# Optimization experiments

Hardware: AMD Instinct MI355X
Metric: run time of the kernel (lower is better)

Reference implementation:

```python
import jax, jax.numpy as jnp
import numpy as np
from jax import lax

BETA = 0.9   # membrane decay
THR = 1.0    # firing threshold (soft reset)
K = 10       # number of time bins
# spatial pyramid for original_shape=(100,368) under 4 stride-2 SAME convs
HW = [(50, 184), (25, 92), (13, 46), (7, 23)]
CH = [4, 8, 16, 32]


def conv(x, w, b, stride=1):
    y = lax.conv_general_dilated(x, w, (stride, stride), 'SAME',
                                 dimension_numbers=('NCHW', 'OIHW', 'NCHW'))
    return y + b[None, :, None, None]


def spike(u):
    # heaviside forward, sigmoid straight-through surrogate backward
    s = (u > 0.0).astype(u.dtype)
    sg = jax.nn.sigmoid(4.0 * u)
    return sg + lax.stop_gradient(s - sg)


def setup_inputs() -> dict:
    key = jax.random.key(0)
    ks = jax.random.split(key, 12)
    T, B = 1000, 1
    x = jax.random.normal(ks[0], (T, B, 1, 100, 368), jnp.float32)

    def w(k, o, i, kh=3, kw=3):
        return 0.1 * jax.random.normal(k, (o, i, kh, kw), jnp.float32)

    inp = {'x': x}
    cin = [1] + CH[:3]
    for li in range(4):
        inp['w%d' % (li + 1)] = w(ks[1 + li], CH[li], cin[li])
        inp['b%d' % (li + 1)] = jnp.zeros((CH[li],), jnp.float32)
    sc = [2 * K * c for c in CH]  # skip channels: [80,160,320,640]
    inp['dw4'] = w(ks[5], 64, sc[3]); inp['db4'] = jnp.zeros((64,), jnp.float32)
    inp['dw3'] = w(ks[6], 32, 64 + sc[2]); inp['db3'] = jnp.zeros((32,), jnp.float32)
    inp['dw2'] = w(ks[7], 16, 32 + sc[1]); inp['db2'] = jnp.zeros((16,), jnp.float32)
    inp['dw1'] = w(ks[8], 8, 16 + sc[0]); inp['db1'] = jnp.zeros((8,), jnp.float32)
    inp['wo'] = w(ks[9], 1, 8, 1, 1); inp['bo'] = jnp.zeros((1,), jnp.float32)
    inp['total_steps'] = 1000
    inp['block_size'] = 100
    return inp


def reference(x, w1, b1, w2, b2, w3, b3, w4, b4,
              dw4, db4, dw3, db3, dw2, db2, dw1, db1, wo, bo,
              total_steps, block_size):
    S = total_steps // K  # steps per bin
    B = x.shape[1]
    xb = x.reshape((K, S) + x.shape[1:])  # [K,S,B,C,H,W]
    mems0 = tuple(jnp.zeros((B, CH[i], HW[i][0], HW[i][1]), x.dtype) for i in range(4))
    enc_w = [(w1, b1), (w2, b2), (w3, b3), (w4, b4)]

    def forward_step(x_t, mems):
        new_mems, spk = [], x_t
        for (wi, bi), m in zip(enc_w, mems):
            m = BETA * m + conv(spk, wi, bi, 2)
            spk = spike(m - THR)
            m = m - spk * THR  # soft reset
            new_mems.append(m)
        return tuple(new_mems)

    def step(carry, x_t):
        mems, sums, sqs = carry
        mems = forward_step(x_t, mems)
        sums = tuple(s + m for s, m in zip(sums, mems))
        sqs = tuple(q + m * m for q, m in zip(sqs, mems))
        return (mems, sums, sqs), None

    def bin_fn(mems, x_bin):
        zeros = tuple(jnp.zeros_like(m) for m in mems)
        (mems, sums, sqs), _ = lax.scan(step, (mems, zeros, zeros), x_bin)
        means = tuple(s / S for s in sums)
        stds = tuple(jnp.sqrt(jnp.maximum(q / S - mu * mu, 1e-8))
                     for q, mu in zip(sqs, means))
        return mems, (means, stds)

    _, (means, stds) = lax.scan(bin_fn, mems0, xb)  # each leaf: [K,B,C,H,W]

    def skip(mean, std):
        # torch.cat([mean0,std0,mean1,std1,...], dim=1) channel ordering
        f = jnp.stack([mean, std], axis=1)        # [K,2,B,C,H,W]
        f = jnp.transpose(f, (2, 0, 1, 3, 4, 5))  # [B,K,2,C,H,W]
        b_, k_, t_, c_, h_, w_ = f.shape
        return f.reshape(b_, k_ * t_ * c_, h_, w_)

    skips = [skip(means[i], stds[i]) for i in range(4)]

    def up(t, hw):
        return jax.image.resize(t, (t.shape[0], t.shape[1], hw[0], hw[1]), 'bilinear')

    relu = jax.nn.relu
    d = relu(conv(skips[3], dw4, db4))
    d = relu(conv(jnp.concatenate([up(d, HW[2]), skips[2]], 1), dw3, db3))
    d = relu(conv(jnp.concatenate([up(d, HW[1]), skips[1]], 1), dw2, db2))
    d = relu(conv(jnp.concatenate([up(d, HW[0]), skips[0]], 1), dw1, db1))
    tau_c = conv(up(d, (100, 368)), wo, bo)  # [B,1,100,368]
    return tau_c
```

## Files before the change

kernel.cpp:

```cpp
#include <hip/hip_runtime.h>

#define KBINS  10
#define SBIN   100
#define BETA   0.9f
#define THR    1.0f
#define CDIV(a,b) (((a)+(b)-1)/(b))

__global__ void k_conv1(const float* __restrict__ x,
                        const float* __restrict__ w1,
                        const float* __restrict__ b1,
                        float* __restrict__ c1) {
    int n = blockIdx.x * blockDim.x + threadIdx.x;
    if (n >= SBIN * 9200) return;
    int w   = n % 184;
    int tmp = n / 184;
    int h   = tmp % 50;
    int t   = tmp / 50;

    const float* xt = x + (size_t)t * 36800;
    float tap[9];
    #pragma unroll
    for (int kh = 0; kh < 3; kh++) {
        int r = 2 * h + kh;
        bool rok = (r < 100);
        int rc = rok ? r : 99;
        #pragma unroll
        for (int kw = 0; kw < 3; kw++) {
            int cc = 2 * w + kw;
            bool cok = (cc < 368);
            int ccc = cok ? cc : 367;
            float v = xt[rc * 368 + ccc];
            tap[kh * 3 + kw] = (rok && cok) ? v : 0.0f;
        }
    }
    float* ot = c1 + (size_t)t * 36800 + h * 184 + w;
    #pragma unroll
    for (int c = 0; c < 4; c++) {
        float acc = b1[c];
        #pragma unroll
        for (int j = 0; j < 9; j++)
            acc = fmaf(tap[j], w1[c * 9 + j], acc);
        ot[c * 9200] = acc;
    }
}

__global__ void k_scan1(const float* __restrict__ c1,
                        float* __restrict__ mstate,
                        unsigned char* __restrict__ spk,
                        float* __restrict__ skip0, int k) {
    const int PF = 10;
    int p = blockIdx.x * blockDim.x + threadIdx.x;
    if (p >= 36800) return;
    int c  = p / 9200;
    int hw = p - c * 9200;

    float m = (k == 0) ? 0.0f : mstate[p];
    float va[PF], vb[PF];
    #pragma unroll
    for (int j = 0; j < PF; j++) va[j] = c1[(size_t)j * 36800 + p];

    float s = 0.0f, q = 0.0f;
    for (int b = 0; b < SBIN / PF; b++) {
        int t0 = b * PF, tn = t0 + PF;
        bool more = (tn < SBIN);
        #pragma unroll
        for (int j = 0; j < PF; j++)
            vb[j] = more ? c1[(size_t)(tn + j) * 36800 + p] : 0.0f;
        #pragma unroll
        for (int j = 0; j < PF; j++) {
            m = fmaf(m, BETA, va[j]);
            float sp = (m - THR > 0.0f) ? 1.0f : 0.0f;
            m -= sp * THR;
            spk[(size_t)(t0 + j) * 36800 + p] = (unsigned char)sp;
            s += m;
            q = fmaf(m, m, q);
        }
        #pragma unroll
        for (int j = 0; j < PF; j++) va[j] = vb[j];
    }
    mstate[p] = m;
    float mean = s * (1.0f / SBIN);
    float var  = q * (1.0f / SBIN) - mean * mean;
    float sd   = sqrtf(fmaxf(var, 1e-8f));
    skip0[(size_t)(k * 8 + c) * 9200 + hw]     = mean;
    skip0[(size_t)(k * 8 + 4 + c) * 9200 + hw] = sd;
}

template<int CIN, int COUT, int HIN, int WIN, int HOUT, int WOUT, int PADH, int PADW>
__global__ void k_conv_s2_multi(const unsigned char* __restrict__ spk_in,
                                const float* __restrict__ wt,
                                const float* __restrict__ bias,
                                float* __restrict__ out) {
    const int total = 1000 * HOUT * WOUT;
    int n = blockIdx.x * blockDim.x + threadIdx.x;
    if (n >= total) return;
    int w   = n % WOUT;
    int tmp = n / WOUT;
    int h   = tmp % HOUT;
    int t   = tmp / HOUT;

    int off[9]; float msk[9];
    #pragma unroll
    for (int kh = 0; kh < 3; kh++) {
        int r = 2 * h + kh - PADH;
        bool rok = (r >= 0) && (r < HIN);
        int rc = rok ? r : 0;
        #pragma unroll
        for (int kw = 0; kw < 3; kw++) {
            int cc = 2 * w + kw - PADW;
            bool cok = (cc >= 0) && (cc < WIN);
            int ccc = cok ? cc : 0;
            off[kh * 3 + kw] = rc * WIN + ccc;
            msk[kh * 3 + kw] = (rok && cok) ? 1.0f : 0.0f;
        }
    }

    float acc[COUT];
    #pragma unroll
    for (int co = 0; co < COUT; co++) acc[co] = bias[co];

    const unsigned char* in_t = spk_in + (size_t)t * (CIN * HIN * WIN);
    for (int ci = 0; ci < CIN; ci++) {
        const unsigned char* ic = in_t + ci * HIN * WIN;
        float tap[9];
        #pragma unroll
        for (int j = 0; j < 9; j++)
            tap[j] = msk[j] * (float)ic[off[j]];
        const float* wci = wt + ci * 9;
        #pragma unroll
        for (int co = 0; co < COUT; co++) {
            #pragma unroll
            for (int j = 0; j < 9; j++)
                acc[co] = fmaf(tap[j], wci[(size_t)co * CIN * 9 + j], acc[co]);
        }
    }
    float* ot = out + (size_t)t * (COUT * HOUT * WOUT) + h * WOUT + w;
    #pragma unroll
    for (int co = 0; co < COUT; co++) ot[co * HOUT * WOUT] = acc[co];
}

__global__ void k_scan(const float* __restrict__ cbuf,
                       unsigned char* __restrict__ spk_out,
                       float* __restrict__ skip,
                       int C, int HW, int write_spk) {
    const int PF = 10;
    int CHW = C * HW;
    int p = blockIdx.x * blockDim.x + threadIdx.x;
    if (p >= CHW) return;
    int c  = p / HW;
    int hw = p - c * HW;

    float m = 0.0f;
    float va[PF], vb[PF];
    #pragma unroll
    for (int j = 0; j < PF; j++) va[j] = cbuf[(size_t)j * CHW + p];

    for (int k = 0; k < KBINS; k++) {
        float s = 0.0f, q = 0.0f;
        for (int b = 0; b < SBIN / PF; b++) {
            int t0 = k * SBIN + b * PF;
            int tn = t0 + PF;
            bool more = (tn < KBINS * SBIN);
            #pragma unroll
            for (int j = 0; j < PF; j++)
                vb[j] = more ? cbuf[(size_t)(tn + j) * CHW + p] : 0.0f;
            #pragma unroll
            for (int j = 0; j < PF; j++) {
                m = fmaf(m, BETA, va[j]);
                float sp = (m - THR > 0.0f) ? 1.0f : 0.0f;
                m -= sp * THR;
                if (write_spk) spk_out[(size_t)(t0 + j) * CHW + p] = (unsigned char)sp;
                s += m;
                q = fmaf(m, m, q);
            }
            #pragma unroll
            for (int j = 0; j < PF; j++) va[j] = vb[j];
        }
        float mean = s * (1.0f / SBIN);
        float var  = q * (1.0f / SBIN) - mean * mean;
        float sd   = sqrtf(fmaxf(var, 1e-8f));
        skip[(size_t)(k * 2 * C + c) * HW + hw]     = mean;
        skip[(size_t)(k * 2 * C + C + c) * HW + hw] = sd;
    }
}

__global__ void k_conv_part(const float* __restrict__ in, int Cin, int H, int W,
                            const float* __restrict__ wt,
                            float* __restrict__ part,
                            int Cout, int CS) {
    int HW  = H * W;
    int pix = blockIdx.x * blockDim.x + threadIdx.x;
    if (pix >= HW) return;
    int co    = blockIdx.y;
    int chunk = blockIdx.z;
    int h = pix / W, w = pix - h * W;

    int off[9]; float msk[9];
    #pragma unroll
    for (int kh = 0; kh < 3; kh++) {
        int r = h + kh - 1;
        bool rok = (r >= 0) && (r < H);
        int rc = rok ? r : 0;
        #pragma unroll
        for (int kw = 0; kw < 3; kw++) {
            int cc = w + kw - 1;
            bool cok = (cc >= 0) && (cc < W);
            int ccc = cok ? cc : 0;
            off[kh * 3 + kw] = rc * W + ccc;
            msk[kh * 3 + kw] = (rok && cok) ? 1.0f : 0.0f;
        }
    }

    const float* ibase = in + (size_t)chunk * CS * HW;
    const float* wbase = wt + ((size_t)co * Cin + (size_t)chunk * CS) * 9;
    float acc = 0.0f;
    #pragma unroll 2
    for (int ci = 0; ci < CS; ci++) {
        const float* ic = ibase + (size_t)ci * HW;
        const float* wc = wbase + ci * 9;
        #pragma unroll
        for (int j = 0; j < 9; j++)
            acc = fmaf(msk[j] * ic[off[j]], wc[j], acc);
    }
    part[((size_t)chunk * Cout + co) * HW + pix] = acc;
}

__global__ void k_reduce_relu(const float* __restrict__ part,
                              const float* __restrict__ bias,
                              float* __restrict__ out,
                              int Cout, int HW, int nchunks) {
    int n = blockIdx.x * blockDim.x + threadIdx.x;
    if (n >= Cout * HW) return;
    int co = n / HW;
    float acc = bias[co];
    for (int c = 0; c < nchunks; c++)
        acc += part[(size_t)c * Cout * HW + n];
    out[n] = fmaxf(acc, 0.0f);
}

__global__ void k_up_cat(const float* __restrict__ up_src, int Cup, int Hi, int Wi,
                         const float* __restrict__ skip, int Cskip,
                         float* __restrict__ out, int Ho, int Wo) {
    int total = (Cup + Cskip) * Ho * Wo;
    int n = blockIdx.x * blockDim.x + threadIdx.x;
    if (n >= total) return;
    int w   = n % Wo;
    int tmp = n / Wo;
    int h   = tmp % Ho;
    int c   = tmp / Ho;
    float v;
    if (c < Cup) {
        float ph = (h + 0.5f) * (float)Hi / (float)Ho - 0.5f;
        float pw = (w + 0.5f) * (float)Wi / (float)Wo - 0.5f;
        float fh = floorf(ph), fw = floorf(pw);
        int h0 = (int)fh, w0 = (int)fw;
        float ah = ph - fh, aw = pw - fw;
        int h0c = min(max(h0, 0), Hi - 1), h1c = min(max(h0 + 1, 0), Hi - 1);
        int w0c = min(max(w0, 0), Wi - 1), w1c = min(max(w0 + 1, 0), Wi - 1);
        const float* sc = up_src + (size_t)c * Hi * Wi;
        float v00 = sc[h0c * Wi + w0c], v01 = sc[h0c * Wi + w1c];
        float v10 = sc[h1c * Wi + w0c], v11 = sc[h1c * Wi + w1c];
        v = (1.0f - ah) * ((1.0f - aw) * v00 + aw * v01)
          + ah * ((1.0f - aw) * v10 + aw * v11);
    } else {
        v = skip[(size_t)(c - Cup) * Ho * Wo + h * Wo + w];
    }
    out[n] = v;
}

__global__ void k_final(const float* __restrict__ d1,
                        const float* __restrict__ wo,
                        const float* __restrict__ bo,
                        float* __restrict__ out) {
    int n = blockIdx.x * blockDim.x + threadIdx.x;
    if (n >= 36800) return;
    int w = n % 368, h = n / 368;
    float ph = (h + 0.5f) * 0.5f - 0.5f;
    float pw = (w + 0.5f) * 0.5f - 0.5f;
    float fh = floorf(ph), fw = floorf(pw);
    int h0 = (int)fh, w0 = (int)fw;
    float ah = ph - fh, aw = pw - fw;
    int h0c = min(max(h0, 0), 49),  h1c = min(max(h0 + 1, 0), 49);
    int w0c = min(max(w0, 0), 183), w1c = min(max(w0 + 1, 0), 183);
    float acc = bo[0];
    #pragma unroll
    for (int c = 0; c < 8; c++) {
        const float* sc = d1 + c * 9200;
        float v00 = sc[h0c * 184 + w0c], v01 = sc[h0c * 184 + w1c];
        float v10 = sc[h1c * 184 + w0c], v11 = sc[h1c * 184 + w1c];
        float v = (1.0f - ah) * ((1.0f - aw) * v00 + aw * v01)
                + ah * ((1.0f - aw) * v10 + aw * v11);
        acc = fmaf(wo[c], v, acc);
    }
    out[n] = acc;
}

extern "C" void kernel_launch(void* const* d_in, const int* in_sizes, int n_in,
                              void* d_out, int out_size, void* d_ws, size_t ws_size,
                              hipStream_t stream) {
    (void)in_sizes; (void)n_in; (void)out_size; (void)ws_size;
    const float* x   = (const float*)d_in[0];
    const float* w1  = (const float*)d_in[1];
    const float* b1  = (const float*)d_in[2];
    const float* w2  = (const float*)d_in[3];
    const float* b2  = (const float*)d_in[4];
    const float* w3  = (const float*)d_in[5];
    const float* b3  = (const float*)d_in[6];
    const float* w4  = (const float*)d_in[7];
    const float* b4  = (const float*)d_in[8];
    const float* dw4 = (const float*)d_in[9];
    const float* db4 = (const float*)d_in[10];
    const float* dw3 = (const float*)d_in[11];
    const float* db3 = (const float*)d_in[12];
    const float* dw2 = (const float*)d_in[13];
    const float* db2 = (const float*)d_in[14];
    const float* dw1 = (const float*)d_in[15];
    const float* db1 = (const float*)d_in[16];
    const float* wo  = (const float*)d_in[17];
    const float* bo  = (const float*)d_in[18];
    float* out = (float*)d_out;

    char* ws = (char*)d_ws;
    size_t off = 0;
    auto alloc = [&](size_t bytes) -> void* {
        void* p = ws + off;
        off += (bytes + 255) & ~(size_t)255;
        return p;
    };
    float*         c1      = (float*)alloc(14720000);
    float*         mstate1 = (float*)alloc(147200);
    unsigned char* spk1    = (unsigned char*)alloc(36800000);
    float*         cbuf    = (float*)alloc(73600000);
    float*         skip0   = (float*)alloc(2944000);
    float*         skip1   = (float*)alloc(1472000);
    float*         skip2   = (float*)alloc(765440);
    float*         skip3   = (float*)alloc(412160);
    unsigned char* spk2 = spk1;
    unsigned char* spk3 = spk1 + 18400000;
    char* dec = (char*)c1;
    size_t doff = 0;
    auto dalloc = [&](size_t bytes) -> void* {
        void* p = dec + doff;
        doff += (bytes + 255) & ~(size_t)255;
        return p;
    };
    float* d4   = (float*)dalloc(10304u * 4);
    float* cat3 = (float*)dalloc(229632u * 4);
    float* d3   = (float*)dalloc(19136u * 4);
    float* cat2 = (float*)dalloc(441600u * 4);
    float* d2   = (float*)dalloc(36800u * 4);
    float* cat1 = (float*)dalloc(883200u * 4);
    float* d1   = (float*)dalloc(73600u * 4);
    float* part = (float*)dalloc(1048576u);

    const int BS = 256;
    const int SBS = 64;

    for (int k = 0; k < KBINS; k++) {
        k_conv1<<<CDIV(SBIN * 9200, BS), BS, 0, stream>>>(
            x + (size_t)k * SBIN * 36800, w1, b1, c1);
        k_scan1<<<CDIV(36800, SBS), SBS, 0, stream>>>(
            c1, mstate1, spk1 + (size_t)k * SBIN * 36800, skip0, k);
    }

    k_conv_s2_multi<4, 8, 50, 184, 25, 92, 0, 0>
        <<<CDIV(1000 * 25 * 92, BS), BS, 0, stream>>>(spk1, w2, b2, cbuf);
    k_scan<<<CDIV(18400, SBS), SBS, 0, stream>>>(cbuf, spk2, skip1, 8, 2300, 1);

    k_conv_s2_multi<8, 16, 25, 92, 13, 46, 1, 0>
        <<<CDIV(1000 * 13 * 46, BS), BS, 0, stream>>>(spk2, w3, b3, cbuf);
    k_scan<<<CDIV(9568, SBS), SBS, 0, stream>>>(cbuf, spk3, skip2, 16, 598, 1);

    k_conv_s2_multi<16, 32, 13, 46, 7, 23, 1, 0>
        <<<CDIV(1000 * 7 * 23, BS), BS, 0, stream>>>(spk3, w4, b4, cbuf);
    k_scan<<<CDIV(5152, SBS), SBS, 0, stream>>>(cbuf, (unsigned char*)cat1 ,
                                                skip3, 32, 161, 0);

    {
        dim3 g(CDIV(161, BS), 64, 10);
        k_conv_part<<<g, BS, 0, stream>>>(skip3, 640, 7, 23, dw4, part, 64, 64);
        k_reduce_relu<<<CDIV(64 * 161, BS), BS, 0, stream>>>(part, db4, d4, 64, 161, 10);
    }
    k_up_cat<<<CDIV(384 * 598, BS), BS, 0, stream>>>(d4, 64, 7, 23,
                                                     skip2, 320, cat3, 13, 46);
    {
        dim3 g(CDIV(598, BS), 32, 8);
        k_conv_part<<<g, BS, 0, stream>>>(cat3, 384, 13, 46, dw3, part, 32, 48);
        k_reduce_relu<<<CDIV(32 * 598, BS), BS, 0, stream>>>(part, db3, d3, 32, 598, 8);
    }
    k_up_cat<<<CDIV(192 * 2300, BS), BS, 0, stream>>>(d3, 32, 13, 46,
                                                      skip1, 160, cat2, 25, 92);
    {
        dim3 g(CDIV(2300, BS), 16, 4);
        k_conv_part<<<g, BS, 0, stream>>>(cat2, 192, 25, 92, dw2, part, 16, 48);
        k_reduce_relu<<<CDIV(16 * 2300, BS), BS, 0, stream>>>(part, db2, d2, 16, 2300, 4);
    }
    k_up_cat<<<CDIV(96 * 9200, BS), BS, 0, stream>>>(d2, 16, 25, 92,
                                                     skip0, 80, cat1, 50, 184);
    {
        dim3 g(CDIV(9200, BS), 8, 2);
        k_conv_part<<<g, BS, 0, stream>>>(cat1, 96, 50, 184, dw1, part, 8, 48);
        k_reduce_relu<<<CDIV(8 * 9200, BS), BS, 0, stream>>>(part, db1, d1, 8, 9200, 2);
    }
    k_final<<<CDIV(36800, BS), BS, 0, stream>>>(d1, wo, bo, out);
}
```

Before: 985.7 us.

## Pad spike buffers, process all timesteps of layer 1 at once, multi-output convs

Spike maps are now written into zero-padded buffers, so the stride-2 convs can load taps without bounds checks or masks. Layer 1 runs as one conv over all 1000 timesteps plus one scan, replacing the 10-bin loop of 20 launches and the membrane state carry. Each conv thread now computes several output columns (and, for conv1, all 4 channels) from shared input taps and writes them with vector stores. The cost is a larger workspace and an extra kernel that zeroes the padded spike buffers.

```diff
diff --git a/kernel.cpp b/kernel.cpp
--- a/kernel.cpp
+++ b/kernel.cpp
@@ -6,149 +6,80 @@
 #define THR    1.0f
 #define CDIV(a,b) (((a)+(b)-1)/(b))
 
+
+__global__ void k_zero16(float4* __restrict__ p, int n16) {
+    int i = blockIdx.x * blockDim.x + threadIdx.x;
+    if (i < n16) p[i] = make_float4(0.f, 0.f, 0.f, 0.f);
+}
+
 __global__ void k_conv1(const float* __restrict__ x,
                         const float* __restrict__ w1,
                         const float* __restrict__ b1,
                         float* __restrict__ c1) {
     int n = blockIdx.x * blockDim.x + threadIdx.x;
-    if (n >= SBIN * 9200) return;
-    int w   = n % 184;
-    int tmp = n / 184;
+    if (n >= 1000 * 50 * 46) return;
+    int wq  = n % 46;
+    int tmp = n / 46;
     int h   = tmp % 50;
     int t   = tmp / 50;
+    int w0  = wq * 4;
 
     const float* xt = x + (size_t)t * 36800;
-    float tap[9];
-    #pragma unroll
-    for (int kh = 0; kh < 3; kh++) {
-        int r = 2 * h + kh;
-        bool rok = (r < 100);
-        int rc = rok ? r : 99;
-        #pragma unroll
-        for (int kw = 0; kw < 3; kw++) {
-            int cc = 2 * w + kw;
-            bool cok = (cc < 368);
-            int ccc = cok ? cc : 367;
-            float v = xt[rc * 368 + ccc];
-            tap[kh * 3 + kw] = (rok && cok) ? v : 0.0f;
+    float rm2 = (h  < 49)  ? 1.f : 0.f;
+    float cm8 = (w0 < 180) ? 1.f : 0.f;
+    int   r2  = min(2 * h + 2, 99);
+    int   cb  = 2 * w0;
+    int   c8  = min(cb + 8, 367);
+
+    const float* row0 = xt + (2 * h) * 368 + cb;
+    const float* row1 = row0 + 368;
+    const float* row2 = xt + r2 * 368 + cb;
+
+    float tap[3][9];
+    #pragma unroll
+    for (int j = 0; j < 8; j++) {
+        tap[0][j] = row0[j];
+        tap[1][j] = row1[j];
+        tap[2][j] = row2[j] * rm2;
+    }
+    tap[0][8] = xt[(2 * h) * 368 + c8] * cm8;
+    tap[1][8] = xt[(2 * h + 1) * 368 + c8] * cm8;
+    tap[2][8] = xt[r2 * 368 + c8] * (rm2 * cm8);
+
+    float* ot = c1 + (size_t)t * 36800 + h * 184 + w0;
+    #pragma unroll
+    for (int co = 0; co < 4; co++) {
+        float b = b1[co];
+        float a0 = b, a1 = b, a2 = b, a3 = b;
+        #pragma unroll
+        for (int r = 0; r < 3; r++) {
+            #pragma unroll
+            for (int kw = 0; kw < 3; kw++) {
+                float wv = w1[co * 9 + r * 3 + kw];
+                a0 = fmaf(tap[r][0 + kw], wv, a0);
+                a1 = fmaf(tap[r][2 + kw], wv, a1);
+                a2 = fmaf(tap[r][4 + kw], wv, a2);
+                a3 = fmaf(tap[r][6 + kw], wv, a3);
+            }
         }
-    }
-    float* ot = c1 + (size_t)t * 36800 + h * 184 + w;
-    #pragma unroll
-    for (int c = 0; c < 4; c++) {
-        float acc = b1[c];
-        #pragma unroll
-        for (int j = 0; j < 9; j++)
-            acc = fmaf(tap[j], w1[c * 9 + j], acc);
-        ot[c * 9200] = acc;
-    }
-}
-
-__global__ void k_scan1(const float* __restrict__ c1,
-                        float* __restrict__ mstate,
-                        unsigned char* __restrict__ spk,
-                        float* __restrict__ skip0, int k) {
-    const int PF = 10;
-    int p = blockIdx.x * blockDim.x + threadIdx.x;
-    if (p >= 36800) return;
-    int c  = p / 9200;
-    int hw = p - c * 9200;
-
-    float m = (k == 0) ? 0.0f : mstate[p];
-    float va[PF], vb[PF];
-    #pragma unroll
-    for (int j = 0; j < PF; j++) va[j] = c1[(size_t)j * 36800 + p];
-
-    float s = 0.0f, q = 0.0f;
-    for (int b = 0; b < SBIN / PF; b++) {
-        int t0 = b * PF, tn = t0 + PF;
-        bool more = (tn < SBIN);
-        #pragma unroll
-        for (int j = 0; j < PF; j++)
-            vb[j] = more ? c1[(size_t)(tn + j) * 36800 + p] : 0.0f;
-        #pragma unroll
-        for (int j = 0; j < PF; j++) {
-            m = fmaf(m, BETA, va[j]);
-            float sp = (m - THR > 0.0f) ? 1.0f : 0.0f;
-            m -= sp * THR;
-            spk[(size_t)(t0 + j) * 36800 + p] = (unsigned char)sp;
-            s += m;
-            q = fmaf(m, m, q);
-        }
-        #pragma unroll
-        for (int j = 0; j < PF; j++) va[j] = vb[j];
-    }
-    mstate[p] = m;
-    float mean = s * (1.0f / SBIN);
-    float var  = q * (1.0f / SBIN) - mean * mean;
-    float sd   = sqrtf(fmaxf(var, 1e-8f));
-    skip0[(size_t)(k * 8 + c) * 9200 + hw]     = mean;
-    skip0[(size_t)(k * 8 + 4 + c) * 9200 + hw] = sd;
-}
-
-template<int CIN, int COUT, int HIN, int WIN, int HOUT, int WOUT, int PADH, int PADW>
-__global__ void k_conv_s2_multi(const unsigned char* __restrict__ spk_in,
-                                const float* __restrict__ wt,
-                                const float* __restrict__ bias,
-                                float* __restrict__ out) {
-    const int total = 1000 * HOUT * WOUT;
-    int n = blockIdx.x * blockDim.x + threadIdx.x;
-    if (n >= total) return;
-    int w   = n % WOUT;
-    int tmp = n / WOUT;
-    int h   = tmp % HOUT;
-    int t   = tmp / HOUT;
-
-    int off[9]; float msk[9];
-    #pragma unroll
-    for (int kh = 0; kh < 3; kh++) {
-        int r = 2 * h + kh - PADH;
-        bool rok = (r >= 0) && (r < HIN);
-        int rc = rok ? r : 0;
-        #pragma unroll
-        for (int kw = 0; kw < 3; kw++) {
-            int cc = 2 * w + kw - PADW;
-            bool cok = (cc >= 0) && (cc < WIN);
-            int ccc = cok ? cc : 0;
-            off[kh * 3 + kw] = rc * WIN + ccc;
-            msk[kh * 3 + kw] = (rok && cok) ? 1.0f : 0.0f;
-        }
-    }
-
-    float acc[COUT];
-    #pragma unroll
-    for (int co = 0; co < COUT; co++) acc[co] = bias[co];
-
-    const unsigned char* in_t = spk_in + (size_t)t * (CIN * HIN * WIN);
-    for (int ci = 0; ci < CIN; ci++) {
-        const unsigned char* ic = in_t + ci * HIN * WIN;
-        float tap[9];
-        #pragma unroll
-        for (int j = 0; j < 9; j++)
-            tap[j] = msk[j] * (float)ic[off[j]];
-        const float* wci = wt + ci * 9;
-        #pragma unroll
-        for (int co = 0; co < COUT; co++) {
-            #pragma unroll
-            for (int j = 0; j < 9; j++)
-                acc[co] = fmaf(tap[j], wci[(size_t)co * CIN * 9 + j], acc[co]);
-        }
-    }
-    float* ot = out + (size_t)t * (COUT * HOUT * WOUT) + h * WOUT + w;
-    #pragma unroll
-    for (int co = 0; co < COUT; co++) ot[co * HOUT * WOUT] = acc[co];
+        *(float4*)(ot + (size_t)co * 9200) = make_float4(a0, a1, a2, a3);
+    }
 }
 
 __global__ void k_scan(const float* __restrict__ cbuf,
-                       unsigned char* __restrict__ spk_out,
+                       unsigned char* __restrict__ spk,
                        float* __restrict__ skip,
-                       int C, int HW, int write_spk) {
+                       int C, int HW, int Win, int Wp, int HpWp, int write_spk) {
     const int PF = 10;
     int CHW = C * HW;
     int p = blockIdx.x * blockDim.x + threadIdx.x;
     if (p >= CHW) return;
     int c  = p / HW;
     int hw = p - c * HW;
+    int h  = hw / Win, w = hw - h * Win;
+
+    unsigned char* sp = spk + (size_t)c * HpWp + (h + 1) * Wp + (w + 1);
+    const size_t tstr = (size_t)C * HpWp;
 
     float m = 0.0f;
     float va[PF], vb[PF];
@@ -167,9 +98,9 @@
             #pragma unroll
             for (int j = 0; j < PF; j++) {
                 m = fmaf(m, BETA, va[j]);
-                float sp = (m - THR > 0.0f) ? 1.0f : 0.0f;
-                m -= sp * THR;
-                if (write_spk) spk_out[(size_t)(t0 + j) * CHW + p] = (unsigned char)sp;
+                float spv = (m - THR > 0.0f) ? 1.0f : 0.0f;
+                m -= spv * THR;
+                if (write_spk) sp[(size_t)(t0 + j) * tstr] = (unsigned char)spv;
                 s += m;
                 q = fmaf(m, m, q);
             }
@@ -181,6 +112,68 @@
         float sd   = sqrtf(fmaxf(var, 1e-8f));
         skip[(size_t)(k * 2 * C + c) * HW + hw]     = mean;
         skip[(size_t)(k * 2 * C + C + c) * HW + hw] = sd;
+    }
+}
+
+template<int CIN, int COUT, int COG, int OW,
+         int HOUT, int WOUT, int PADH, int HP, int WP>
+__global__ void k_convs2(const unsigned char* __restrict__ spk,
+                         const float* __restrict__ wt,
+                         const float* __restrict__ bias,
+                         float* __restrict__ out) {
+    const int WQ = (WOUT + OW - 1) / OW;
+    const int NT = 2 * OW + 1;
+    int n = blockIdx.x * blockDim.x + threadIdx.x;
+    if (n >= 1000 * HOUT * WQ) return;
+    int wq  = n % WQ;
+    int tmp = n / WQ;
+    int h   = tmp % HOUT;
+    int t   = tmp / HOUT;
+    int cog = blockIdx.y;
+    int w0  = wq * OW;
+
+    const unsigned char* base = spk + (size_t)t * CIN * HP * WP
+                              + (2 * h - PADH + 1) * WP + (2 * w0 + 1);
+
+    float acc[OW][COG];
+    #pragma unroll
+    for (int q = 0; q < OW; q++)
+        #pragma unroll
+        for (int co = 0; co < COG; co++) acc[q][co] = bias[cog * COG + co];
+
+    for (int ci = 0; ci < CIN; ci++) {
+        const unsigned char* ic = base + (size_t)ci * HP * WP;
+        float tap[3][NT];
+        #pragma unroll
+        for (int r = 0; r < 3; r++)
+            #pragma unroll
+            for (int j = 0; j < NT; j++)
+                tap[r][j] = (float)ic[r * WP + j];
+        #pragma unroll
+        for (int co = 0; co < COG; co++) {
+            const float* wc = wt + ((size_t)(cog * COG + co) * CIN + ci) * 9;
+            #pragma unroll
+            for (int r = 0; r < 3; r++)
+                #pragma unroll
+                for (int kw = 0; kw < 3; kw++) {
+                    float wv = wc[r * 3 + kw];
+                    #pragma unroll
+                    for (int q = 0; q < OW; q++)
+                        acc[q][co] = fmaf(tap[r][2 * q + kw], wv, acc[q][co]);
+                }
+        }
+    }
+
+    float* ot = out + ((size_t)t * COUT + cog * COG) * (HOUT * WOUT) + h * WOUT + w0;
+    #pragma unroll
+    for (int co = 0; co < COG; co++) {
+        float* oc = ot + (size_t)co * (HOUT * WOUT);
+        if constexpr (OW == 4) {
+            *(float4*)oc = make_float4(acc[0][co], acc[1][co], acc[2][co], acc[3][co]);
+        } else {
+            if (w0 + 2 <= WOUT) *(float2*)oc = make_float2(acc[0][co], acc[1][co]);
+            else                oc[0] = acc[0][co];
+        }
     }
 }
 
@@ -327,17 +320,15 @@
         off += (bytes + 255) & ~(size_t)255;
         return p;
     };
-    float*         c1      = (float*)alloc(14720000);
-    float*         mstate1 = (float*)alloc(147200);
-    unsigned char* spk1    = (unsigned char*)alloc(36800000);
-    float*         cbuf    = (float*)alloc(73600000);
-    float*         skip0   = (float*)alloc(2944000);
-    float*         skip1   = (float*)alloc(1472000);
-    float*         skip2   = (float*)alloc(765440);
-    float*         skip3   = (float*)alloc(412160);
-    unsigned char* spk2 = spk1;
-    unsigned char* spk3 = spk1 + 18400000;
-    char* dec = (char*)c1;
+    float*         cbuf  = (float*)alloc(147200000);
+    unsigned char* spk1p = (unsigned char*)alloc(39936000);
+    unsigned char* spk2p = (unsigned char*)alloc(21600000);
+    unsigned char* spk3p = (unsigned char*)alloc(12960000);
+    float*         skip0 = (float*)alloc(2944000);
+    float*         skip1 = (float*)alloc(1472000);
+    float*         skip2 = (float*)alloc(765440);
+    float*         skip3 = (float*)alloc(412160);
+    char* dec = (char*)cbuf;
     size_t doff = 0;
     auto dalloc = [&](size_t bytes) -> void* {
         void* p = dec + doff;
@@ -353,28 +344,32 @@
     float* d1   = (float*)dalloc(73600u * 4);
     float* part = (float*)dalloc(1048576u);
 
-    const int BS = 256;
+    const int BS  = 256;
     const int SBS = 64;
 
-    for (int k = 0; k < KBINS; k++) {
-        k_conv1<<<CDIV(SBIN * 9200, BS), BS, 0, stream>>>(
-            x + (size_t)k * SBIN * 36800, w1, b1, c1);
-        k_scan1<<<CDIV(36800, SBS), SBS, 0, stream>>>(
-            c1, mstate1, spk1 + (size_t)k * SBIN * 36800, skip0, k);
-    }
-
-    k_conv_s2_multi<4, 8, 50, 184, 25, 92, 0, 0>
-        <<<CDIV(1000 * 25 * 92, BS), BS, 0, stream>>>(spk1, w2, b2, cbuf);
-    k_scan<<<CDIV(18400, SBS), SBS, 0, stream>>>(cbuf, spk2, skip1, 8, 2300, 1);
-
-    k_conv_s2_multi<8, 16, 25, 92, 13, 46, 1, 0>
-        <<<CDIV(1000 * 13 * 46, BS), BS, 0, stream>>>(spk2, w3, b3, cbuf);
-    k_scan<<<CDIV(9568, SBS), SBS, 0, stream>>>(cbuf, spk3, skip2, 16, 598, 1);
-
-    k_conv_s2_multi<16, 32, 13, 46, 7, 23, 1, 0>
-        <<<CDIV(1000 * 7 * 23, BS), BS, 0, stream>>>(spk3, w4, b4, cbuf);
-    k_scan<<<CDIV(5152, SBS), SBS, 0, stream>>>(cbuf, (unsigned char*)cat1 ,
-                                                skip3, 32, 161, 0);
+    {
+        int n16 = (39936000 + 21600000 + 12960000) / 16;
+        k_zero16<<<CDIV(n16, BS), BS, 0, stream>>>((float4*)spk1p, n16);
+    }
+
+    k_conv1<<<CDIV(1000 * 50 * 46, BS), BS, 0, stream>>>(x, w1, b1, cbuf);
+    k_scan<<<CDIV(36800, SBS), SBS, 0, stream>>>(cbuf, spk1p, skip0,
+                                                 4, 9200, 184, 192, 52 * 192, 1);
+
+    k_convs2<4, 8, 8, 4, 25, 92, 0, 52, 192>
+        <<<dim3(CDIV(1000 * 25 * 23, BS), 1), BS, 0, stream>>>(spk1p, w2, b2, cbuf);
+    k_scan<<<CDIV(18400, SBS), SBS, 0, stream>>>(cbuf, spk2p, skip1,
+                                                 8, 2300, 92, 100, 27 * 100, 1);
+
+    k_convs2<8, 16, 16, 2, 13, 46, 1, 27, 100>
+        <<<dim3(CDIV(1000 * 13 * 23, BS), 1), BS, 0, stream>>>(spk2p, w3, b3, cbuf);
+    k_scan<<<CDIV(9568, SBS), SBS, 0, stream>>>(cbuf, spk3p, skip2,
+                                                16, 598, 46, 54, 15 * 54, 1);
+
+    k_convs2<16, 32, 16, 2, 7, 23, 1, 15, 54>
+        <<<dim3(CDIV(1000 * 7 * 12, BS), 2), BS, 0, stream>>>(spk3p, w4, b4, cbuf);
+    k_scan<<<CDIV(5152, SBS), SBS, 0, stream>>>(cbuf, spk3p , skip3,
+                                                32, 161, 23, 31, 9 * 31, 0);
 
     {
         dim3 g(CDIV(161, BS), 64, 10);
```

Result: no change. 1.001 ms (+1.6%).
